# Optimization experiments

Hardware: AMD Instinct MI355X
Metric: run time of the kernel (lower is better)

## Reference

```python
import jax, jax.numpy as jnp
import numpy as np

L, H, E, HS, T, B, V = 6, 12, 768, 64, 1024, 2, 32000
EPS = 1e-5


def layer_norm(x, g, b):
    mu = jnp.mean(x, axis=-1, keepdims=True)
    var = jnp.mean(jnp.square(x - mu), axis=-1, keepdims=True)
    return (x - mu) * jax.lax.rsqrt(var + EPS) * g + b


def setup_inputs() -> dict:
    key = jax.random.key(0)
    ks = jax.random.split(key, 24)
    s = 0.02
    inp = {
        "idx": jax.random.randint(ks[0], (B, T), 0, V),
        "targets": jax.random.randint(ks[1], (B, T), 0, V),
        "tok_emb": jax.random.normal(ks[2], (V, E), jnp.float32) * s,
        "pos_emb": jax.random.normal(ks[3], (T, E), jnp.float32) * s,
        "ln1_g": jnp.ones((L, E), jnp.float32),
        "ln1_b": jnp.zeros((L, E), jnp.float32),
        "wq": jax.random.normal(ks[4], (L, E, E), jnp.float32) * s,
        "wk": jax.random.normal(ks[5], (L, E, E), jnp.float32) * s,
        "wv": jax.random.normal(ks[6], (L, E, E), jnp.float32) * s,
        "wproj": jax.random.normal(ks[7], (L, E, E), jnp.float32) * s,
        "bproj": jnp.zeros((L, E), jnp.float32),
        "ln2_g": jnp.ones((L, E), jnp.float32),
        "ln2_b": jnp.zeros((L, E), jnp.float32),
        "w1": jax.random.normal(ks[8], (L, E, 4 * E), jnp.float32) * s,
        "b1": jnp.zeros((L, 4 * E), jnp.float32),
        "w2": jax.random.normal(ks[9], (L, 4 * E, E), jnp.float32) * s,
        "b2": jnp.zeros((L, E), jnp.float32),
        "lnf_g": jnp.ones((E,), jnp.float32),
        "lnf_b": jnp.zeros((E,), jnp.float32),
        "lm_w": jax.random.normal(ks[10], (E, V), jnp.float32) * s,
        "lm_b": jnp.zeros((V,), jnp.float32),
    }
    return inp


def reference(idx, targets, tok_emb, pos_emb, ln1_g, ln1_b, wq, wk, wv, wproj,
              bproj, ln2_g, ln2_b, w1, b1, w2, b2, lnf_g, lnf_b, lm_w, lm_b):
    x = tok_emb[idx] + pos_emb[None, :T, :]  # [B,T,E]
    causal = jnp.tril(jnp.ones((T, T), bool))
    scale = E ** (-0.5)  # NOTE: original scales by n_embed**-0.5, not head_size
    for l in range(L):
        h = layer_norm(x, ln1_g[l], ln1_b[l])
        q = (h @ wq[l]).reshape(B, T, H, HS)
        k = (h @ wk[l]).reshape(B, T, H, HS)
        v = (h @ wv[l]).reshape(B, T, H, HS)
        scores = jnp.einsum('bqhd,bkhd->bhqk', q, k) * scale
        scores = jnp.where(causal[None, None], scores, -jnp.inf)
        w = jax.nn.softmax(scores, axis=-1)
        attn = jnp.einsum('bhqk,bkhd->bqhd', w, v).reshape(B, T, E)
        # original MultiHeadAttention applies proj TWICE (faithful reproduction)
        out = attn @ wproj[l] + bproj[l]
        out = out @ wproj[l] + bproj[l]
        x = x + out
        h2 = layer_norm(x, ln2_g[l], ln2_b[l])
        x = x + (jax.nn.relu(h2 @ w1[l] + b1[l]) @ w2[l] + b2[l])
    x = layer_norm(x, lnf_g, lnf_b)
    logits = x @ lm_w + lm_b  # [B,T,V]
    logp = jax.nn.log_softmax(logits, axis=-1)
    nll = -jnp.take_along_axis(logp, targets[..., None], axis=-1)[..., 0]
    loss = jnp.mean(nll)
    return logits, loss
```

## Files before the change

### kernel.cpp

```cpp
#include <hip/hip_runtime.h>
#include <math.h>

#define NL 6
#define NH 12
#define NE 768
#define NHS 64
#define NT 1024
#define NB 2
#define NV 32000
#define NM (NB * NT)
#define NQKV (3 * NE)
#define NFF (4 * NE)
#define LN_EPS 1e-5f

typedef __attribute__((ext_vector_type(8))) short short8;
typedef __attribute__((ext_vector_type(4))) float f32x4;
typedef __attribute__((ext_vector_type(4))) unsigned short ushort4v;
typedef __attribute__((address_space(1))) const unsigned int as1_cuint;
typedef __attribute__((address_space(3))) unsigned int as3_uint;

__device__ __forceinline__ unsigned short f2bf(float f) {
    unsigned int u = __builtin_bit_cast(unsigned int, f);
    u += 0x7fffu + ((u >> 16) & 1u);
    return (unsigned short)(u >> 16);
}
__device__ __forceinline__ float bf2f(unsigned short u) {
    unsigned int v = ((unsigned int)u) << 16;
    return __builtin_bit_cast(float, v);
}
__device__ __forceinline__ void gload_lds16(const void* g, void* l) {
    __builtin_amdgcn_global_load_lds((as1_cuint*)g, (as3_uint*)l, 16, 0, 0);
}

__global__ __launch_bounds__(256) void embed_ln_kernel(const int* __restrict__ idx,
                                                       const float* __restrict__ tok,
                                                       const float* __restrict__ pos,
                                                       const float* __restrict__ g,
                                                       const float* __restrict__ b,
                                                       float* __restrict__ x,
                                                       unsigned short* __restrict__ hbuf) {
    __shared__ float red[256];
    int row = blockIdx.x, tid = threadIdx.x;
    int t = row % NT;
    int id = idx[row];
    float v[3]; float s = 0.f;
    #pragma unroll
    for (int k = 0; k < 3; ++k) {
        int c = tid + k * 256;
        v[k] = tok[(long)id * NE + c] + pos[(long)t * NE + c];
        x[(long)row * NE + c] = v[k];
        s += v[k];
    }
    red[tid] = s; __syncthreads();
    for (int o = 128; o > 0; o >>= 1) { if (tid < o) red[tid] += red[tid + o]; __syncthreads(); }
    float mu = red[0] / NE;
    __syncthreads();
    float vr = 0.f;
    #pragma unroll
    for (int k = 0; k < 3; ++k) { float d = v[k] - mu; vr += d * d; }
    red[tid] = vr; __syncthreads();
    for (int o = 128; o > 0; o >>= 1) { if (tid < o) red[tid] += red[tid + o]; __syncthreads(); }
    float rstd = rsqrtf(red[0] / NE + LN_EPS);
    #pragma unroll
    for (int k = 0; k < 3; ++k) {
        int c = tid + k * 256;
        hbuf[(long)row * NE + c] = f2bf((v[k] - mu) * rstd * g[c] + b[c]);
    }
}

template<int S>
__global__ __launch_bounds__(256) void combine_ln_kernel(const float* __restrict__ parts,
                                                         const float* __restrict__ bias,
                                                         float* __restrict__ x,
                                                         const float* __restrict__ g,
                                                         const float* __restrict__ b,
                                                         unsigned short* __restrict__ hbuf) {
    __shared__ float red[256];
    int row = blockIdx.x, tid = threadIdx.x;
    float v[3]; float s = 0.f;
    #pragma unroll
    for (int k = 0; k < 3; ++k) {
        int c = tid + k * 256;
        long i = (long)row * NE + c;
        float a = parts[i];
        #pragma unroll
        for (int si = 1; si < S; ++si) a += parts[(long)si * NM * NE + i];
        a += bias[c] + x[i];
        x[i] = a;
        v[k] = a; s += a;
    }
    red[tid] = s; __syncthreads();
    for (int o = 128; o > 0; o >>= 1) { if (tid < o) red[tid] += red[tid + o]; __syncthreads(); }
    float mu = red[0] / NE;
    __syncthreads();
    float vr = 0.f;
    #pragma unroll
    for (int k = 0; k < 3; ++k) { float d = v[k] - mu; vr += d * d; }
    red[tid] = vr; __syncthreads();
    for (int o = 128; o > 0; o >>= 1) { if (tid < o) red[tid] += red[tid + o]; __syncthreads(); }
    float rstd = rsqrtf(red[0] / NE + LN_EPS);
    #pragma unroll
    for (int k = 0; k < 3; ++k) {
        int c = tid + k * 256;
        hbuf[(long)row * NE + c] = f2bf((v[k] - mu) * rstd * g[c] + b[c]);
    }
}

__global__ __launch_bounds__(256) void transpose4b_kernel(const float* __restrict__ wq,
                                                          const float* __restrict__ wk,
                                                          const float* __restrict__ wv,
                                                          const float* __restrict__ wp,
                                                          unsigned short* __restrict__ wqkvT,
                                                          unsigned short* __restrict__ wprojT) {
    __shared__ float t[32][33];
    int z = blockIdx.z, l = z >> 2, which = z & 3;
    const float* W = ((which == 0) ? wq : (which == 1) ? wk : (which == 2) ? wv : wp) + (long)l * NE * NE;
    unsigned short* WT = (which < 3) ? (wqkvT + (long)l * NQKV * NE + (long)which * NE * NE)
                                     : (wprojT + (long)l * NE * NE);
    int k0 = blockIdx.y * 32, n0 = blockIdx.x * 32;
    int c = threadIdx.x & 31, r = threadIdx.x >> 5;
    #pragma unroll
    for (int p = 0; p < 4; ++p)
        t[r + p * 8][c] = W[(long)(k0 + r + p * 8) * NE + n0 + c];
    __syncthreads();
    #pragma unroll
    for (int p = 0; p < 4; ++p)
        WT[(long)(n0 + r + p * 8) * NE + k0 + c] = f2bf(t[c][r + p * 8]);
}

__global__ __launch_bounds__(256) void transpose_cast_b_kernel(const float* __restrict__ W0,
                                                               unsigned short* __restrict__ WT0,
                                                               int K, int N) {
    __shared__ float t[32][33];
    long lofs = (long)blockIdx.z * K * N;
    const float* W = W0 + lofs;
    unsigned short* WT = WT0 + lofs;
    int k0 = blockIdx.y * 32, n0 = blockIdx.x * 32;
    int c = threadIdx.x & 31, r = threadIdx.x >> 5;
    #pragma unroll
    for (int p = 0; p < 4; ++p)
        t[r + p * 8][c] = W[(long)(k0 + r + p * 8) * N + n0 + c];
    __syncthreads();
    #pragma unroll
    for (int p = 0; p < 4; ++p)
        WT[(long)(n0 + r + p * 8) * K + k0 + c] = f2bf(t[c][r + p * 8]);
}

__global__ __launch_bounds__(256) void cast_kernel(const float* __restrict__ W,
                                                   unsigned short* __restrict__ O, long n) {
    long i = ((long)blockIdx.x * 256 + threadIdx.x) * 4;
    if (i < n) {
        float4 v = *(const float4*)(W + i);
        ushort4v o;
        o[0] = f2bf(v.x); o[1] = f2bf(v.y); o[2] = f2bf(v.z); o[3] = f2bf(v.w);
        *(ushort4v*)(O + i) = o;
    }
}

__global__ __launch_bounds__(256) void beff_b_kernel(const float* __restrict__ bproj,
                                                     const unsigned short* __restrict__ wprojT,
                                                     float* __restrict__ beff) {
    __shared__ float red[256];
    int n = blockIdx.x, l = blockIdx.y, tid = threadIdx.x;
    const unsigned short* wp = wprojT + (long)l * NE * NE + (long)n * NE;
    const float* bp = bproj + (long)l * NE;
    float acc = 0.f;
    for (int j = tid; j < NE; j += 256) acc += bp[j] * bf2f(wp[j]);
    red[tid] = acc; __syncthreads();
    for (int o = 128; o > 0; o >>= 1) { if (tid < o) red[tid] += red[tid + o]; __syncthreads(); }
    if (tid == 0) beff[(long)l * NE + n] = red[0] + bp[n];
}

template<int S>
__global__ __launch_bounds__(256) void combine_kernel(const float* __restrict__ parts,
                                                      unsigned short* __restrict__ bout,
                                                      long total) {
    long i = ((long)blockIdx.x * 256 + threadIdx.x) * 4;
    if (i >= total) return;
    float4 a = *(const float4*)(parts + i);
    #pragma unroll
    for (int s = 1; s < S; ++s) {
        float4 b = *(const float4*)(parts + (long)s * total + i);
        a.x += b.x; a.y += b.y; a.z += b.z; a.w += b.w;
    }
    ushort4v o;
    o[0] = f2bf(a.x); o[1] = f2bf(a.y); o[2] = f2bf(a.z); o[3] = f2bf(a.w);
    *(ushort4v*)(bout + i) = o;
}

template<typename OutT, bool BIAS, bool RELU, int SPLITK>
__global__ __launch_bounds__(256) void gemm_mfma(const unsigned short* __restrict__ A,
                                                 const unsigned short* __restrict__ BT,
                                                 const float* __restrict__ bias,
                                                 OutT* __restrict__ C,
                                                 int gridM, int N, int K) {
    __shared__ unsigned short As[2][128 * 32];
    __shared__ unsigned short Bs[2][128 * 32];
    int tid = threadIdx.x;
    int lane = tid & 63, w = tid >> 6;
    int wr = w >> 1, wc = w & 1;
    int l4 = lane >> 4, l15 = lane & 15;

    int nwg = gridDim.x, orig = blockIdx.x;
    int q = nwg >> 3, r8 = nwg & 7;
    int xcd = orig & 7, ii = orig >> 3;
    int wg = (xcd < r8) ? (xcd * (q + 1) + ii) : (r8 * (q + 1) + (xcd - r8) * q + ii);
    int bm = wg % gridM, bn = wg / gridM;
    int m0 = bm * 128, n0 = bn * 128;

    int kb = K / SPLITK;
    int koff = (SPLITK > 1) ? blockIdx.y * kb : 0;

    f32x4 acc[4][4] = {};

    int srow = lane >> 2;
    int scol = (lane & 3) * 8;

    #pragma unroll
    for (int it = 0; it < 2; ++it) {
        int rr = w * 32 + it * 16;
        gload_lds16(&A [(long)(m0 + rr + srow) * K + koff + scol], &As[0][rr * 32]);
        gload_lds16(&BT[(long)(n0 + rr + srow) * K + koff + scol], &Bs[0][rr * 32]);
    }

    int cur = 0;
    for (int k0 = 0; k0 < kb; k0 += 32) {
        __syncthreads();
        if (k0 + 32 < kb) {
            #pragma unroll
            for (int it = 0; it < 2; ++it) {
                int rr = w * 32 + it * 16;
                gload_lds16(&A [(long)(m0 + rr + srow) * K + koff + k0 + 32 + scol], &As[cur ^ 1][rr * 32]);
                gload_lds16(&BT[(long)(n0 + rr + srow) * K + koff + k0 + 32 + scol], &Bs[cur ^ 1][rr * 32]);
            }
        }

        short8 a[4], b[4];
        #pragma unroll
        for (int f = 0; f < 4; ++f) {
            a[f] = *(const short8*)&As[cur][(wr * 64 + f * 16 + l15) * 32 + l4 * 8];
            b[f] = *(const short8*)&Bs[cur][(wc * 64 + f * 16 + l15) * 32 + l4 * 8];
        }
        __builtin_amdgcn_s_setprio(1);
        #pragma unroll
        for (int fm = 0; fm < 4; ++fm)
            #pragma unroll
            for (int fn = 0; fn < 4; ++fn)
                acc[fm][fn] = __builtin_amdgcn_mfma_f32_16x16x32_bf16(a[fm], b[fn], acc[fm][fn], 0, 0, 0);
        __builtin_amdgcn_s_setprio(0);
        cur ^= 1;
    }

    if constexpr (SPLITK > 1) {
        float* Cp = (float*)C + (long)blockIdx.y * gridM * 128 * N;
        #pragma unroll
        for (int fm = 0; fm < 4; ++fm)
            #pragma unroll
            for (int j = 0; j < 4; ++j) {
                long row = m0 + wr * 64 + fm * 16 + l4 * 4 + j;
                #pragma unroll
                for (int fn = 0; fn < 4; ++fn)
                    Cp[row * N + n0 + wc * 64 + fn * 16 + l15] = acc[fm][fn][j];
            }
    } else {
        float bs[4];
        #pragma unroll
        for (int fn = 0; fn < 4; ++fn)
            bs[fn] = BIAS ? bias[n0 + wc * 64 + fn * 16 + l15] : 0.f;

        #pragma unroll
        for (int fm = 0; fm < 4; ++fm) {
            #pragma unroll
            for (int j = 0; j < 4; ++j) {
                long row = m0 + wr * 64 + fm * 16 + l4 * 4 + j;
                #pragma unroll
                for (int fn = 0; fn < 4; ++fn) {
                    int col = n0 + wc * 64 + fn * 16 + l15;
                    float v = acc[fm][fn][j] + bs[fn];
                    if (RELU) v = fmaxf(v, 0.f);
                    if constexpr (sizeof(OutT) == 2) C[row * N + col] = (OutT)f2bf(v);
                    else                             C[row * N + col] = v;
                }
            }
        }
    }
}

__global__ __launch_bounds__(256) void gemm_weff_kernel(const unsigned short* __restrict__ A0,
                                                        const unsigned short* __restrict__ B0,
                                                        unsigned short* __restrict__ C0,
                                                        int gridM, int N, int K) {
    __shared__ unsigned short As[2][128 * 32];
    __shared__ unsigned short Bs[2][128 * 32];
    long zofs = (long)blockIdx.z * N * K;
    const unsigned short* A = A0 + zofs;
    const unsigned short* BT = B0 + zofs;
    unsigned short* C = C0 + zofs;
    int tid = threadIdx.x;
    int lane = tid & 63, w = tid >> 6;
    int wr = w >> 1, wc = w & 1;
    int l4 = lane >> 4, l15 = lane & 15;
    int bm = blockIdx.x % gridM, bn = blockIdx.x / gridM;
    int m0 = bm * 128, n0 = bn * 128;

    f32x4 acc[4][4] = {};
    int srow = lane >> 2;
    int scol = (lane & 3) * 8;

    #pragma unroll
    for (int it = 0; it < 2; ++it) {
        int rr = w * 32 + it * 16;
        gload_lds16(&A [(long)(m0 + rr + srow) * K + scol], &As[0][rr * 32]);
        gload_lds16(&BT[(long)(n0 + rr + srow) * K + scol], &Bs[0][rr * 32]);
    }
    int cur = 0;
    for (int k0 = 0; k0 < K; k0 += 32) {
        __syncthreads();
        if (k0 + 32 < K) {
            #pragma unroll
            for (int it = 0; it < 2; ++it) {
                int rr = w * 32 + it * 16;
                gload_lds16(&A [(long)(m0 + rr + srow) * K + k0 + 32 + scol], &As[cur ^ 1][rr * 32]);
                gload_lds16(&BT[(long)(n0 + rr + srow) * K + k0 + 32 + scol], &Bs[cur ^ 1][rr * 32]);
            }
        }
        short8 a[4], b[4];
        #pragma unroll
        for (int f = 0; f < 4; ++f) {
            a[f] = *(const short8*)&As[cur][(wr * 64 + f * 16 + l15) * 32 + l4 * 8];
            b[f] = *(const short8*)&Bs[cur][(wc * 64 + f * 16 + l15) * 32 + l4 * 8];
        }
        #pragma unroll
        for (int fm = 0; fm < 4; ++fm)
            #pragma unroll
            for (int fn = 0; fn < 4; ++fn)
                acc[fm][fn] = __builtin_amdgcn_mfma_f32_16x16x32_bf16(a[fm], b[fn], acc[fm][fn], 0, 0, 0);
        cur ^= 1;
    }
    #pragma unroll
    for (int fm = 0; fm < 4; ++fm)
        #pragma unroll
        for (int j = 0; j < 4; ++j) {
            long row = m0 + wr * 64 + fm * 16 + l4 * 4 + j;
            #pragma unroll
            for (int fn = 0; fn < 4; ++fn)
                C[row * N + n0 + wc * 64 + fn * 16 + l15] = f2bf(acc[fm][fn][j]);
        }
}

__global__ __launch_bounds__(512, 2) void gemm256_lse(const unsigned short* __restrict__ A,
                                                      const unsigned short* __restrict__ BT,
                                                      const float* __restrict__ bias,
                                                      float* __restrict__ C,
                                                      float* __restrict__ pm, float* __restrict__ ps,
                                                      int gridM, int N, int K) {
    __shared__ unsigned short Al[4][256 * 32];
    __shared__ unsigned short Bl[4][256 * 32];
    int tid = threadIdx.x;
    int lane = tid & 63, w = tid >> 6;
    int wr = w >> 2, wn = w & 3;
    int l4 = lane >> 4, l15 = lane & 15;

    int nwg = gridDim.x, orig = blockIdx.x;
    int q = nwg >> 3, r8 = nwg & 7;
    int xcd = orig & 7, ii = orig >> 3;
    int wg = (xcd < r8) ? (xcd * (q + 1) + ii) : (r8 * (q + 1) + (xcd - r8) * q + ii);
    int bm = wg % gridM, bn = wg / gridM;
    int m0 = bm * 256, n0 = bn * 256;

    int nkt = K >> 5;

    int srow = lane >> 2;
    int sslot = (lane & 3) ^ ((lane >> 3) & 3);

    auto STAGE = [&](int slot, int kt) {
        #pragma unroll
        for (int it = 0; it < 2; ++it) {
            int r0 = (w * 2 + it) * 16;
            gload_lds16(&A [(long)(m0 + r0 + srow) * K + kt * 32 + sslot * 8], &Al[slot][r0 * 32]);
            gload_lds16(&BT[(long)(n0 + r0 + srow) * K + kt * 32 + sslot * 8], &Bl[slot][r0 * 32]);
        }
    };

    f32x4 acc[8][4] = {};
    int rsw = (l4 ^ ((l15 >> 1) & 3)) * 8;

    STAGE(0, 0);
    STAGE(1, 1);

    for (int t = 0; t < nkt; ++t) {
        if (t + 2 < nkt) STAGE((t + 2) & 3, t + 2);
        int ahead = nkt - 1 - t;
        if (ahead >= 2)      asm volatile("s_waitcnt vmcnt(8)" ::: "memory");
        else if (ahead == 1) asm volatile("s_waitcnt vmcnt(4)" ::: "memory");
        else                 asm volatile("s_waitcnt vmcnt(0)" ::: "memory");
        asm volatile("s_barrier" ::: "memory");

        int s = t & 3;
        short8 af[8], bf[4];
        #pragma unroll
        for (int f = 0; f < 8; ++f)
            af[f] = *(const short8*)&Al[s][(wr * 128 + f * 16 + l15) * 32 + rsw];
        #pragma unroll
        for (int f = 0; f < 4; ++f)
            bf[f] = *(const short8*)&Bl[s][(wn * 64 + f * 16 + l15) * 32 + rsw];

        __builtin_amdgcn_s_setprio(1);
        #pragma unroll
        for (int fm = 0; fm < 8; ++fm)
            #pragma unroll
            for (int fn = 0; fn < 4; ++fn)
                acc[fm][fn] = __builtin_amdgcn_mfma_f32_16x16x32_bf16(af[fm], bf[fn], acc[fm][fn], 0, 0, 0);
        __builtin_amdgcn_s_setprio(0);
    }

    float bs[4];
    #pragma unroll
    for (int fn = 0; fn < 4; ++fn)
        bs[fn] = bias[n0 + wn * 64 + fn * 16 + l15];

    #pragma unroll
    for (int fm = 0; fm < 8; ++fm) {
        #pragma unroll
        for (int j = 0; j < 4; ++j) {
            long row = m0 + wr * 128 + fm * 16 + l4 * 4 + j;
            float v4[4];
            #pragma unroll
            for (int fn = 0; fn < 4; ++fn) {
                int col = n0 + wn * 64 + fn * 16 + l15;
                float v = acc[fm][fn][j] + bs[fn];
                C[row * N + col] = v;
                v4[fn] = v;
            }
            float mx = fmaxf(fmaxf(v4[0], v4[1]), fmaxf(v4[2], v4[3]));
            #pragma unroll
            for (int off = 1; off < 16; off <<= 1) mx = fmaxf(mx, __shfl_xor(mx, off));
            float sm = 0.f;
            #pragma unroll
            for (int fn = 0; fn < 4; ++fn) sm += __expf(v4[fn] - mx);
            #pragma unroll
            for (int off = 1; off < 16; off <<= 1) sm += __shfl_xor(sm, off);
            if (l15 == 0) {
                int pidx = bn * 4 + wn;
                pm[row * 512 + pidx] = mx;
                ps[row * 512 + pidx] = sm;
            }
        }
    }
}

__global__ __launch_bounds__(256) void vtrans_kernel(const unsigned short* __restrict__ qkv,
                                                     unsigned short* __restrict__ vt) {
    __shared__ unsigned short t[64][72];
    int t0 = blockIdx.x * 64;
    int bh = blockIdx.y;
    int b = bh / NH, h = bh % NH;
    int tid = threadIdx.x;
    #pragma unroll
    for (int i = 0; i < 2; ++i) {
        int r = (tid >> 3) + i * 32, c8 = (tid & 7) * 8;
        short8 v = *(const short8*)(qkv + ((long)b * NT + t0 + r) * NQKV + 2 * NE + h * NHS + c8);
        *(short8*)&t[r][c8] = v;
    }
    __syncthreads();
    #pragma unroll
    for (int i = 0; i < 2; ++i) {
        int d = (tid >> 3) + i * 32, s = (tid & 7) * 8;
        short8 o;
        #pragma unroll
        for (int j = 0; j < 8; ++j) o[j] = (short)t[s + j][d];
        *(short8*)(vt + ((long)bh * NHS + d) * NT + t0 + s) = o;
    }
}

__global__ __launch_bounds__(256) void fattn_kernel(const unsigned short* __restrict__ qkv,
                                                    const unsigned short* __restrict__ vt,
                                                    unsigned short* __restrict__ out) {
    __shared__ unsigned short Ks[2][64 * 64];
    __shared__ unsigned short Vl[2][64 * 64];
    __shared__ unsigned short Ps[4 * 16 * 64];
    int qt = gridDim.x - 1 - blockIdx.x;
    int bh = blockIdx.y;
    int b = bh / NH, h = bh % NH;
    int tid = threadIdx.x, lane = tid & 63, w = tid >> 6;
    int l4 = lane >> 4, l15 = lane & 15;
    long rowb = (long)b * NT;
    const float scale = 0.03608439182435161f;
    const unsigned short* vtp = vt + (long)bh * NHS * NT;

    const unsigned short* qptr = qkv + (rowb + qt * 64 + w * 16 + l15) * NQKV + h * NHS;
    short8 qa0 = *(const short8*)(qptr + l4 * 8);
    short8 qa1 = *(const short8*)(qptr + 32 + l4 * 8);

    f32x4 o[4] = {};
    float m[4], lsum[4];
    #pragma unroll
    for (int j = 0; j < 4; ++j) { m[j] = -INFINITY; lsum[j] = 0.f; }

    int kr_r = tid >> 3, kr_c = (tid & 7) * 8;
    int vr_d = tid >> 3, vr_s = tid & 7;

    short8 kr[2], vr[2];
    auto LOADT = [&](int t) {
        int kbase = t * 64;
        #pragma unroll
        for (int i = 0; i < 2; ++i) {
            kr[i] = *(const short8*)(qkv + (rowb + kbase + kr_r + i * 32) * NQKV + NE + h * NHS + kr_c);
            vr[i] = *(const short8*)(vtp + (long)(vr_d + i * 32) * NT + kbase + vr_s * 8);
        }
    };

    LOADT(0);
    for (int t = 0; t <= qt; ++t) {
        int cur = t & 1;
        #pragma unroll
        for (int i = 0; i < 2; ++i) {
            int r = kr_r + i * 32;
            *(short8*)&Ks[cur][r * 64 + (kr_c ^ ((r & 7) << 3))] = kr[i];
            int d = vr_d + i * 32;
            *(short8*)&Vl[cur][d * 64 + ((vr_s * 8) ^ ((d & 7) << 3))] = vr[i];
        }
        asm volatile("s_waitcnt lgkmcnt(0)" ::: "memory");
        if (t < qt) LOADT(t + 1);
        asm volatile("s_barrier" ::: "memory");

        f32x4 s[4];
        __builtin_amdgcn_s_setprio(1);
        #pragma unroll
        for (int fn = 0; fn < 4; ++fn) {
            int key = fn * 16 + l15;
            short8 kb0 = *(const short8*)&Ks[cur][key * 64 + ((l4 * 8) ^ ((key & 7) << 3))];
            short8 kb1 = *(const short8*)&Ks[cur][key * 64 + ((32 + l4 * 8) ^ ((key & 7) << 3))];
            f32x4 z = {};
            z = __builtin_amdgcn_mfma_f32_16x16x32_bf16(qa0, kb0, z, 0, 0, 0);
            s[fn] = __builtin_amdgcn_mfma_f32_16x16x32_bf16(qa1, kb1, z, 0, 0, 0);
        }
        __builtin_amdgcn_s_setprio(0);

        if (t == qt) {
            #pragma unroll
            for (int fn = 0; fn < 4; ++fn) {
                int key = t * 64 + fn * 16 + l15;
                #pragma unroll
                for (int j = 0; j < 4; ++j) {
                    int qrow = qt * 64 + w * 16 + l4 * 4 + j;
                    s[fn][j] = (key <= qrow) ? s[fn][j] * scale : -1e30f;
                }
            }
        } else {
            #pragma unroll
            for (int fn = 0; fn < 4; ++fn)
                #pragma unroll
                for (int j = 0; j < 4; ++j)
                    s[fn][j] *= scale;
        }

        #pragma unroll
        for (int j = 0; j < 4; ++j) {
            float mj = fmaxf(fmaxf(s[0][j], s[1][j]), fmaxf(s[2][j], s[3][j]));
            #pragma unroll
            for (int off = 1; off < 16; off <<= 1) mj = fmaxf(mj, __shfl_xor(mj, off));
            float mnew = fmaxf(m[j], mj);
            float alpha = __expf(m[j] - mnew);
            m[j] = mnew;
            float psum = 0.f;
            #pragma unroll
            for (int fn = 0; fn < 4; ++fn) {
                float p = __expf(s[fn][j] - mnew);
                psum += p;
                int rr = l4 * 4 + j, c = fn * 16 + l15;
                Ps[w * 1024 + rr * 64 + (c ^ ((rr & 7) << 3))] = f2bf(p);
            }
            #pragma unroll
            for (int off = 1; off < 16; off <<= 1) psum += __shfl_xor(psum, off);
            lsum[j] = lsum[j] * alpha + psum;
            #pragma unroll
            for (int fn = 0; fn < 4; ++fn) o[fn][j] *= alpha;
        }

        short8 pa0 = *(const short8*)&Ps[w * 1024 + l15 * 64 + ((l4 * 8) ^ ((l15 & 7) << 3))];
        short8 pa1 = *(const short8*)&Ps[w * 1024 + l15 * 64 + ((32 + l4 * 8) ^ ((l15 & 7) << 3))];
        __builtin_amdgcn_s_setprio(1);
        #pragma unroll
        for (int fn = 0; fn < 4; ++fn) {
            int d = fn * 16 + l15;
            short8 vb0 = *(const short8*)&Vl[cur][d * 64 + ((l4 * 8) ^ ((d & 7) << 3))];
            short8 vb1 = *(const short8*)&Vl[cur][d * 64 + ((32 + l4 * 8) ^ ((d & 7) << 3))];
            o[fn] = __builtin_amdgcn_mfma_f32_16x16x32_bf16(pa0, vb0, o[fn], 0, 0, 0);
            o[fn] = __builtin_amdgcn_mfma_f32_16x16x32_bf16(pa1, vb1, o[fn], 0, 0, 0);
        }
        __builtin_amdgcn_s_setprio(0);
    }

    #pragma unroll
    for (int j = 0; j < 4; ++j) {
        long row = rowb + qt * 64 + w * 16 + l4 * 4 + j;
        float inv = 1.0f / lsum[j];
        #pragma unroll
        for (int fn = 0; fn < 4; ++fn)
            out[row * NE + h * NHS + fn * 16 + l15] = f2bf(o[fn][j] * inv);
    }
}

__global__ __launch_bounds__(256) void nll_combine_kernel(const float* __restrict__ logits,
                                                          const float* __restrict__ pm,
                                                          const float* __restrict__ ps,
                                                          const int* __restrict__ targets,
                                                          float* __restrict__ nll) {
    __shared__ float rm[256], rs[256];
    int row = blockIdx.x, tid = threadIdx.x;
    float m = -1e30f, s = 0.f;
    for (int i = tid; i < 500; i += 256) {
        float m2 = pm[(long)row * 512 + i], s2 = ps[(long)row * 512 + i];
        float mm = fmaxf(m, m2);
        s = s * __expf(m - mm) + s2 * __expf(m2 - mm);
        m = mm;
    }
    rm[tid] = m; rs[tid] = s; __syncthreads();
    for (int o = 128; o > 0; o >>= 1) {
        if (tid < o) {
            float m2 = rm[tid + o], s2 = rs[tid + o];
            float mm = fmaxf(rm[tid], m2);
            rs[tid] = rs[tid] * __expf(rm[tid] - mm) + s2 * __expf(m2 - mm);
            rm[tid] = mm;
        }
        __syncthreads();
    }
    if (tid == 0) {
        int tgt = targets[row];
        nll[row] = -(logits[(long)row * NV + tgt] - rm[0] - logf(rs[0]));
    }
}

__global__ void loss_reduce_kernel(const float* __restrict__ nll, float* __restrict__ out) {
    __shared__ float red[256];
    int tid = threadIdx.x;
    float s = 0.f;
    for (int i = tid; i < NM; i += 256) s += nll[i];
    red[tid] = s; __syncthreads();
    for (int o = 128; o > 0; o >>= 1) { if (tid < o) red[tid] += red[tid + o]; __syncthreads(); }
    if (tid == 0) out[0] = red[0] / NM;
}

extern "C" void kernel_launch(void* const* d_in, const int* in_sizes, int n_in,
                              void* d_out, int out_size, void* d_ws, size_t ws_size,
                              hipStream_t stream) {
    const int*   idx     = (const int*)  d_in[0];
    const int*   targets = (const int*)  d_in[1];
    const float* tok     = (const float*)d_in[2];
    const float* pos     = (const float*)d_in[3];
    const float* ln1_g   = (const float*)d_in[4];
    const float* ln1_b   = (const float*)d_in[5];
    const float* wq      = (const float*)d_in[6];
    const float* wk      = (const float*)d_in[7];
    const float* wv      = (const float*)d_in[8];
    const float* wproj   = (const float*)d_in[9];
    const float* bproj   = (const float*)d_in[10];
    const float* ln2_g   = (const float*)d_in[11];
    const float* ln2_b   = (const float*)d_in[12];
    const float* w1      = (const float*)d_in[13];
    const float* b1      = (const float*)d_in[14];
    const float* w2      = (const float*)d_in[15];
    const float* b2      = (const float*)d_in[16];
    const float* lnf_g   = (const float*)d_in[17];
    const float* lnf_b   = (const float*)d_in[18];
    const float* lm_w    = (const float*)d_in[19];
    const float* lm_b    = (const float*)d_in[20];

    float* logits = (float*)d_out;
    float* loss   = logits + (long)NM * NV;

    char* p = (char*)d_ws;
    float*          x      = (float*)p;          p += (long)NM * NE * 4;
    unsigned short* hbuf   = (unsigned short*)p; p += (long)NM * NE * 2;
    unsigned short* qkv    = (unsigned short*)p; p += (long)NM * NQKV * 2;
    unsigned short* att    = (unsigned short*)p; p += (long)NM * NE * 2;
    unsigned short* hid    = (unsigned short*)p; p += (long)NM * NFF * 2;
    unsigned short* vt     = (unsigned short*)p; p += (long)NB * NH * NHS * NT * 2;
    float*          nll    = (float*)p;          p += (long)NM * 4;
    float*          pmb    = (float*)p;          p += (long)NM * 512 * 4;
    float*          psb    = (float*)p;          p += (long)NM * 512 * 4;
    float*          parts  = (float*)p;          p += (long)2 * NM * NQKV * 4;
    unsigned short* wqkvT6 = (unsigned short*)p; p += (long)NL * NQKV * NE * 2;
    unsigned short* wprojT6= (unsigned short*)p; p += (long)NL * NE * NE * 2;
    unsigned short* wprojC6= (unsigned short*)p; p += (long)NL * NE * NE * 2;
    unsigned short* weffT6 = (unsigned short*)p; p += (long)NL * NE * NE * 2;
    float*          beff6  = (float*)p;          p += (long)NL * NE * 4;
    unsigned short* w1T6   = (unsigned short*)p; p += (long)NL * NFF * NE * 2;
    unsigned short* w2T6   = (unsigned short*)p; p += (long)NL * NE * NFF * 2;
    unsigned short* lmT    = (unsigned short*)p; p += (long)NV * NE * 2;

    dim3 blk(256);

    transpose4b_kernel<<<dim3(NE / 32, NE / 32, 4 * NL), blk, 0, stream>>>(
        wq, wk, wv, wproj, wqkvT6, wprojT6);
    cast_kernel<<<(NL * NE * NE) / 1024, blk, 0, stream>>>(wproj, wprojC6, (long)NL * NE * NE);
    transpose_cast_b_kernel<<<dim3(NFF / 32, NE / 32, NL), blk, 0, stream>>>(w1, w1T6, NE, NFF);
    transpose_cast_b_kernel<<<dim3(NE / 32, NFF / 32, NL), blk, 0, stream>>>(w2, w2T6, NFF, NE);
    gemm_weff_kernel<<<dim3(36, 1, NL), blk, 0, stream>>>(wprojT6, wprojC6, weffT6, 6, NE, NE);
    beff_b_kernel<<<dim3(NE, NL), blk, 0, stream>>>(bproj, wprojT6, beff6);
    transpose_cast_b_kernel<<<dim3(NV / 32, NE / 32, 1), blk, 0, stream>>>(lm_w, lmT, NE, NV);

    embed_ln_kernel<<<NM, blk, 0, stream>>>(idx, tok, pos, ln1_g, ln1_b, x, hbuf);

    for (int l = 0; l < NL; ++l) {
        gemm_mfma<float, false, false, 2><<<dim3((NM/128)*(NQKV/128), 2), blk, 0, stream>>>(
            hbuf, wqkvT6 + (long)l * NQKV * NE, nullptr, parts, NM / 128, NQKV, NE);
        combine_kernel<2><<<(NM * NQKV) / 1024, blk, 0, stream>>>(parts, qkv, (long)NM * NQKV);
        vtrans_kernel<<<dim3(NT / 64, NB * NH), blk, 0, stream>>>(qkv, vt);
        fattn_kernel<<<dim3(NT / 64, NB * NH), blk, 0, stream>>>(qkv, vt, att);
        gemm_mfma<float, false, false, 2><<<dim3((NM/128)*(NE/128), 2), blk, 0, stream>>>(
            att, weffT6 + (long)l * NE * NE, nullptr, parts, NM / 128, NE, NE);
        combine_ln_kernel<2><<<NM, blk, 0, stream>>>(
            parts, beff6 + (long)l * NE, x, ln2_g + (long)l * NE, ln2_b + (long)l * NE, hbuf);
        gemm_mfma<unsigned short, true, true, 1><<<dim3((NM/128)*(NFF/128)), blk, 0, stream>>>(
            hbuf, w1T6 + (long)l * NFF * NE, b1 + (long)l * NFF, hid, NM / 128, NFF, NE);
        gemm_mfma<float, false, false, 4><<<dim3((NM/128)*(NE/128), 4), blk, 0, stream>>>(
            hid, w2T6 + (long)l * NE * NFF, nullptr, parts, NM / 128, NE, NFF);
        const float* ng = (l < NL - 1) ? (ln1_g + (long)(l + 1) * NE) : lnf_g;
        const float* nb = (l < NL - 1) ? (ln1_b + (long)(l + 1) * NE) : lnf_b;
        combine_ln_kernel<4><<<NM, blk, 0, stream>>>(parts, b2 + (long)l * NE, x, ng, nb, hbuf);
    }

    gemm256_lse<<<dim3((NM/256)*(NV/256)), dim3(512), 0, stream>>>(
        hbuf, lmT, lm_b, logits, pmb, psb, NM / 256, NV, NE);
    nll_combine_kernel<<<NM, blk, 0, stream>>>(logits, pmb, psb, targets, nll);
    loss_reduce_kernel<<<1, blk, 0, stream>>>(nll, loss);
}
```

Measured before the change: 1.186 ms.

## Swizzle LDS layout in gemm_mfma kernels and retile LM-head GEMM to 256x128

Applies an XOR swizzle to the LDS staging column and the matching fragment reads in both 128x128 MFMA GEMM kernels, to reduce LDS bank conflicts. The LM-head GEMM changes from a 256x256 tile with a 4-deep pipeline to a 256x128 tile with double buffering and an extra barrier after the fragment loads. This halves per-block LDS and accumulator registers so more blocks can be resident, and it launches twice as many blocks. The trade-off is less data reuse per tile and an extra synchronisation in each k-step. The partial max/sum index now uses 2 slots per column block; with 250 column blocks that is 500 slots, which still fits the 512-wide buffer.

Measured after the change: 1.180 ms. About the same (-0.5%).

```diff
diff --git a/kernel.cpp b/kernel.cpp
--- a/kernel.cpp
+++ b/kernel.cpp
@@ -214,7 +214,8 @@
     f32x4 acc[4][4] = {};
 
     int srow = lane >> 2;
-    int scol = (lane & 3) * 8;
+    int scol = ((lane & 3) ^ ((lane >> 3) & 3)) * 8;
+    int rsw  = (l4 ^ ((l15 >> 1) & 3)) * 8;
 
     #pragma unroll
     for (int it = 0; it < 2; ++it) {
@@ -238,8 +239,8 @@
         short8 a[4], b[4];
         #pragma unroll
         for (int f = 0; f < 4; ++f) {
-            a[f] = *(const short8*)&As[cur][(wr * 64 + f * 16 + l15) * 32 + l4 * 8];
-            b[f] = *(const short8*)&Bs[cur][(wc * 64 + f * 16 + l15) * 32 + l4 * 8];
+            a[f] = *(const short8*)&As[cur][(wr * 64 + f * 16 + l15) * 32 + rsw];
+            b[f] = *(const short8*)&Bs[cur][(wc * 64 + f * 16 + l15) * 32 + rsw];
         }
         __builtin_amdgcn_s_setprio(1);
         #pragma unroll
@@ -305,7 +306,8 @@
 
     f32x4 acc[4][4] = {};
     int srow = lane >> 2;
-    int scol = (lane & 3) * 8;
+    int scol = ((lane & 3) ^ ((lane >> 3) & 3)) * 8;
+    int rsw  = (l4 ^ ((l15 >> 1) & 3)) * 8;
 
     #pragma unroll
     for (int it = 0; it < 2; ++it) {
@@ -327,8 +329,8 @@
         short8 a[4], b[4];
         #pragma unroll
         for (int f = 0; f < 4; ++f) {
-            a[f] = *(const short8*)&As[cur][(wr * 64 + f * 16 + l15) * 32 + l4 * 8];
-            b[f] = *(const short8*)&Bs[cur][(wc * 64 + f * 16 + l15) * 32 + l4 * 8];
+            a[f] = *(const short8*)&As[cur][(wr * 64 + f * 16 + l15) * 32 + rsw];
+            b[f] = *(const short8*)&Bs[cur][(wc * 64 + f * 16 + l15) * 32 + rsw];
         }
         #pragma unroll
         for (int fm = 0; fm < 4; ++fm)
@@ -348,17 +350,17 @@
         }
 }
 
-__global__ __launch_bounds__(512, 2) void gemm256_lse(const unsigned short* __restrict__ A,
-                                                      const unsigned short* __restrict__ BT,
-                                                      const float* __restrict__ bias,
-                                                      float* __restrict__ C,
-                                                      float* __restrict__ pm, float* __restrict__ ps,
-                                                      int gridM, int N, int K) {
-    __shared__ unsigned short Al[4][256 * 32];
-    __shared__ unsigned short Bl[4][256 * 32];
+__global__ __launch_bounds__(512, 4) void gemm256x128_lse(const unsigned short* __restrict__ A,
+                                                          const unsigned short* __restrict__ BT,
+                                                          const float* __restrict__ bias,
+                                                          float* __restrict__ C,
+                                                          float* __restrict__ pm, float* __restrict__ ps,
+                                                          int gridM, int N, int K) {
+    __shared__ unsigned short Al[2][256 * 32];
+    __shared__ unsigned short Bl[2][128 * 32];
     int tid = threadIdx.x;
     int lane = tid & 63, w = tid >> 6;
-    int wr = w >> 2, wn = w & 3;
+    int wm = w >> 1, wn = w & 1;
     int l4 = lane >> 4, l15 = lane & 15;
 
     int nwg = gridDim.x, orig = blockIdx.x;
@@ -366,48 +368,48 @@
     int xcd = orig & 7, ii = orig >> 3;
     int wg = (xcd < r8) ? (xcd * (q + 1) + ii) : (r8 * (q + 1) + (xcd - r8) * q + ii);
     int bm = wg % gridM, bn = wg / gridM;
-    int m0 = bm * 256, n0 = bn * 256;
+    int m0 = bm * 256, n0 = bn * 128;
 
     int nkt = K >> 5;
-
     int srow = lane >> 2;
-    int sslot = (lane & 3) ^ ((lane >> 3) & 3);
+    int sslot = ((lane & 3) ^ ((lane >> 3) & 3)) * 8;
 
     auto STAGE = [&](int slot, int kt) {
         #pragma unroll
-        for (int it = 0; it < 2; ++it) {
-            int r0 = (w * 2 + it) * 16;
-            gload_lds16(&A [(long)(m0 + r0 + srow) * K + kt * 32 + sslot * 8], &Al[slot][r0 * 32]);
-            gload_lds16(&BT[(long)(n0 + r0 + srow) * K + kt * 32 + sslot * 8], &Bl[slot][r0 * 32]);
-        }
+        for (int p = 0; p < 2; ++p) {
+            int r0 = p * 128 + w * 16;
+            gload_lds16(&A[(long)(m0 + r0 + srow) * K + kt * 32 + sslot], &Al[slot][r0 * 32]);
+        }
+        int r0 = w * 16;
+        gload_lds16(&BT[(long)(n0 + r0 + srow) * K + kt * 32 + sslot], &Bl[slot][r0 * 32]);
     };
 
-    f32x4 acc[8][4] = {};
+    f32x4 acc[4][4] = {};
     int rsw = (l4 ^ ((l15 >> 1) & 3)) * 8;
 
     STAGE(0, 0);
-    STAGE(1, 1);
-
     for (int t = 0; t < nkt; ++t) {
-        if (t + 2 < nkt) STAGE((t + 2) & 3, t + 2);
-        int ahead = nkt - 1 - t;
-        if (ahead >= 2)      asm volatile("s_waitcnt vmcnt(8)" ::: "memory");
-        else if (ahead == 1) asm volatile("s_waitcnt vmcnt(4)" ::: "memory");
-        else                 asm volatile("s_waitcnt vmcnt(0)" ::: "memory");
+        if (t + 1 < nkt) {
+            STAGE((t + 1) & 1, t + 1);
+            asm volatile("s_waitcnt vmcnt(3)" ::: "memory");
+        } else {
+            asm volatile("s_waitcnt vmcnt(0)" ::: "memory");
+        }
         asm volatile("s_barrier" ::: "memory");
 
-        int s = t & 3;
-        short8 af[8], bf[4];
-        #pragma unroll
-        for (int f = 0; f < 8; ++f)
-            af[f] = *(const short8*)&Al[s][(wr * 128 + f * 16 + l15) * 32 + rsw];
-        #pragma unroll
-        for (int f = 0; f < 4; ++f)
+        int s = t & 1;
+        short8 af[4], bf[4];
+        #pragma unroll
+        for (int f = 0; f < 4; ++f) {
+            af[f] = *(const short8*)&Al[s][(wm * 64 + f * 16 + l15) * 32 + rsw];
             bf[f] = *(const short8*)&Bl[s][(wn * 64 + f * 16 + l15) * 32 + rsw];
+        }
+        asm volatile("s_waitcnt lgkmcnt(0)" ::: "memory");
+        asm volatile("s_barrier" ::: "memory");
 
         __builtin_amdgcn_s_setprio(1);
         #pragma unroll
-        for (int fm = 0; fm < 8; ++fm)
+        for (int fm = 0; fm < 4; ++fm)
             #pragma unroll
             for (int fn = 0; fn < 4; ++fn)
                 acc[fm][fn] = __builtin_amdgcn_mfma_f32_16x16x32_bf16(af[fm], bf[fn], acc[fm][fn], 0, 0, 0);
@@ -420,10 +422,10 @@
         bs[fn] = bias[n0 + wn * 64 + fn * 16 + l15];
 
     #pragma unroll
-    for (int fm = 0; fm < 8; ++fm) {
+    for (int fm = 0; fm < 4; ++fm) {
         #pragma unroll
         for (int j = 0; j < 4; ++j) {
-            long row = m0 + wr * 128 + fm * 16 + l4 * 4 + j;
+            long row = m0 + wm * 64 + fm * 16 + l4 * 4 + j;
             float v4[4];
             #pragma unroll
             for (int fn = 0; fn < 4; ++fn) {
@@ -441,7 +443,7 @@
             #pragma unroll
             for (int off = 1; off < 16; off <<= 1) sm += __shfl_xor(sm, off);
             if (l15 == 0) {
-                int pidx = bn * 4 + wn;
+                int pidx = bn * 2 + wn;
                 pm[row * 512 + pidx] = mx;
                 ps[row * 512 + pidx] = sm;
             }
@@ -722,7 +724,7 @@
         combine_ln_kernel<4><<<NM, blk, 0, stream>>>(parts, b2 + (long)l * NE, x, ng, nb, hbuf);
     }
 
-    gemm256_lse<<<dim3((NM/256)*(NV/256)), dim3(512), 0, stream>>>(
+    gemm256x128_lse<<<dim3((NM/256)*(NV/128)), dim3(512), 0, stream>>>(
         hbuf, lmT, lm_b, logits, pmb, psb, NM / 256, NV, NE);
     nll_combine_kernel<<<NM, blk, 0, stream>>>(logits, pmb, psb, targets, nll);
     loss_reduce_kernel<<<1, blk, 0, stream>>>(nll, loss);
```
